# Optimization experiments

Measured on AMD Instinct MI355X. Metric: run time of the kernel, lower is better.

The kernel has to match this reference:

```python
import jax, jax.numpy as jnp
import numpy as np

B, S, H = 2, 1024, 4096
NH, NKV, D = 32, 8, 128
EPS = 1e-6
THETA = 10000.0


def rotate_half(x):
    x1, x2 = jnp.split(x, 2, axis=-1)
    return jnp.concatenate([-x2, x1], axis=-1)


def rmsnorm(x, w, eps):
    # RMSNorm over the last (head_dim) axis
    var = jnp.mean(x * x, axis=-1, keepdims=True)
    return x * jax.lax.rsqrt(var + eps) * w


def setup_inputs() -> dict:
    key = jax.random.key(0)
    ks = jax.random.split(key, 6)
    hidden_states = jax.random.normal(ks[0], (B, S, H), dtype=jnp.float32)
    # scaled init so activations stay O(1)
    Wq = jax.random.normal(ks[1], (NH * D, H), dtype=jnp.float32) * (H ** -0.5)
    Wk = jax.random.normal(ks[2], (NKV * D, H), dtype=jnp.float32) * (H ** -0.5)
    Wv = jax.random.normal(ks[3], (NKV * D, H), dtype=jnp.float32) * (H ** -0.5)
    Wo = jax.random.normal(ks[4], (H, NH * D), dtype=jnp.float32) * ((NH * D) ** -0.5)
    q_norm_w = jnp.ones((D,), dtype=jnp.float32)
    k_norm_w = jnp.ones((D,), dtype=jnp.float32)
    # standard default RoPE cos/sin tables, broadcast to [B, S, D]
    pos = jnp.arange(S, dtype=jnp.float32)
    inv_freq = 1.0 / (THETA ** (jnp.arange(0, D, 2, dtype=jnp.float32) / D))
    freqs = pos[:, None] * inv_freq[None, :]            # [S, D/2]
    emb = jnp.concatenate([freqs, freqs], axis=-1)      # [S, D]
    cos = jnp.broadcast_to(jnp.cos(emb)[None], (B, S, D)).astype(jnp.float32)
    sin = jnp.broadcast_to(jnp.sin(emb)[None], (B, S, D)).astype(jnp.float32)
    return dict(hidden_states=hidden_states, cos=cos, sin=sin,
                Wq=Wq, Wk=Wk, Wv=Wv, Wo=Wo,
                q_norm_w=q_norm_w, k_norm_w=k_norm_w)


def reference(hidden_states, cos, sin, Wq, Wk, Wv, Wo, q_norm_w, k_norm_w):
    b, s, h = hidden_states.shape
    # fused QKV projections (MojoLinear: y = x @ W.T, no bias)
    q = (hidden_states @ Wq.T).reshape(b, s, NH, D)
    k = (hidden_states @ Wk.T).reshape(b, s, NKV, D)
    v = (hidden_states @ Wv.T).reshape(b, s, NKV, D)
    # per-head-dim RMSNorm on q and k, then [B, H, S, D] layout
    q = rmsnorm(q, q_norm_w, EPS).transpose(0, 2, 1, 3)   # [B, NH,  S, D]
    k = rmsnorm(k, k_norm_w, EPS).transpose(0, 2, 1, 3)   # [B, NKV, S, D]
    v = v.transpose(0, 2, 1, 3)                           # [B, NKV, S, D]
    # RoPE (rotate-half)
    c = cos[:, None, :, :]
    sn = sin[:, None, :, :]
    q = q * c + rotate_half(q) * sn
    k = k * c + rotate_half(k) * sn
    # GQA: expand KV heads to query heads
    groups = NH // NKV
    k = jnp.repeat(k, groups, axis=1)                     # [B, NH, S, D]
    v = jnp.repeat(v, groups, axis=1)
    # causal attention (prefill with empty paged cache == causal SDPA)
    scores = jnp.einsum('bhqd,bhkd->bhqk', q, k) * (D ** -0.5)
    causal = jnp.tril(jnp.ones((s, s), dtype=bool))
    scores = jnp.where(causal, scores, jnp.finfo(scores.dtype).min)
    probs = jax.nn.softmax(scores, axis=-1)
    out = jnp.einsum('bhqk,bhkd->bhqd', probs, v)         # [B, NH, S, D]
    out = out.transpose(0, 2, 1, 3).reshape(b, s, NH * D)
    return out @ Wo.T
```

## Files before the change

kernel.cpp:

```cpp
#include <hip/hip_runtime.h>


typedef float  f32x4   __attribute__((ext_vector_type(4)));
typedef float  f32x16  __attribute__((ext_vector_type(16)));
typedef __bf16 bf16x8  __attribute__((ext_vector_type(8)));
typedef unsigned short u16x8 __attribute__((ext_vector_type(8)));

__device__ __forceinline__ unsigned short f2b(float f) {
    union { float f; unsigned int u; } x;
    x.f = f;
    unsigned int u = x.u;
    unsigned int r = u + 0x7fffu + ((u >> 16) & 1u);
    return (unsigned short)(r >> 16);
}
__device__ __forceinline__ float b2f(unsigned short h) {
    union { unsigned int u; float f; } x;
    x.u = ((unsigned int)h) << 16;
    return x.f;
}

__device__ __forceinline__ void async16(const unsigned short* g, unsigned short* l) {
    __builtin_amdgcn_global_load_lds(
        (const __attribute__((address_space(1))) void*)g,
        (__attribute__((address_space(3))) void*)l, 16, 0, 0);
}

__global__ __launch_bounds__(256) void cvt_pack(const float* __restrict__ hid,
                                                const float* __restrict__ Wq,
                                                const float* __restrict__ Wk,
                                                const float* __restrict__ Wv,
                                                const float* __restrict__ Wo,
                                                unsigned short* __restrict__ hidb,
                                                unsigned short* __restrict__ Wqkvb,
                                                unsigned short* __restrict__ Wob) {
    __shared__ __align__(16) unsigned short L[8192];
    const int t = threadIdx.x;
    const int tile = blockIdx.x;

    const float* src;
    unsigned short* dst;
    int kb;
    if (tile < 1024) {
        int rb = tile >> 6; kb = tile & 63;
        src = hid + (size_t)rb * 128 * 4096;
        dst = hidb + (size_t)tile * 8192;
    } else if (tile < 4096) {
        int tt = tile - 1024;
        int rb = tt >> 6; kb = tt & 63;
        dst = Wqkvb + (size_t)tt * 8192;
        if (rb < 32)      src = Wq + (size_t)rb * 128 * 4096;
        else if (rb < 40) src = Wk + (size_t)(rb - 32) * 128 * 4096;
        else              src = Wv + (size_t)(rb - 40) * 128 * 4096;
    } else {
        int tt = tile - 4096;
        int rb = tt >> 6; kb = tt & 63;
        src = Wo + (size_t)rb * 128 * 4096;
        dst = Wob + (size_t)tt * 8192;
    }

    const int r0 = t >> 2, cq = t & 3;
    #pragma unroll
    for (int rr = 0; rr < 2; rr++) {
        int row = r0 + rr * 64;
        const float* sp = src + (size_t)row * 4096 + kb * 64 + cq * 16;
        float4 v0 = ((const float4*)sp)[0];
        float4 v1 = ((const float4*)sp)[1];
        float4 v2 = ((const float4*)sp)[2];
        float4 v3 = ((const float4*)sp)[3];
        u16x8 a, b;
        a[0]=f2b(v0.x); a[1]=f2b(v0.y); a[2]=f2b(v0.z); a[3]=f2b(v0.w);
        a[4]=f2b(v1.x); a[5]=f2b(v1.y); a[6]=f2b(v1.z); a[7]=f2b(v1.w);
        b[0]=f2b(v2.x); b[1]=f2b(v2.y); b[2]=f2b(v2.z); b[3]=f2b(v2.w);
        b[4]=f2b(v3.x); b[5]=f2b(v3.y); b[6]=f2b(v3.z); b[7]=f2b(v3.w);
        *(u16x8*)&L[((cq * 2)     * 128 + row) * 8] = a;
        *(u16x8*)&L[((cq * 2 + 1) * 128 + row) * 8] = b;
    }
    __syncthreads();
    #pragma unroll
    for (int j = 0; j < 4; j++)
        *(u16x8*)(dst + t * 32 + j * 8) = *(const u16x8*)&L[t * 32 + j * 8];
}

template<bool BF16OUT>
__global__ __launch_bounds__(256) void gemm_packed(const unsigned short* __restrict__ A,
                                                   const unsigned short* __restrict__ W,
                                                   void* __restrict__ Cv,
                                                   int K, int N) {
    __shared__ __align__(16) unsigned short As[8192];
    __shared__ __align__(16) unsigned short Bs[8192];

    const int tid  = threadIdx.x;
    const int wave = tid >> 6, lane = tid & 63;
    const int wm   = wave >> 1, wn = wave & 1;
    const int l31  = lane & 31, lh = lane >> 5;
    const int KT   = K >> 6;

    const unsigned short* Ap = A + (size_t)blockIdx.y * KT * 8192;
    const unsigned short* Wp = W + (size_t)blockIdx.x * KT * 8192;

    f32x16 acc[2][2] = {};

    for (int kt = 0; kt < KT; kt++) {
        const unsigned short* at = Ap + (size_t)kt * 8192;
        const unsigned short* wt = Wp + (size_t)kt * 8192;
        #pragma unroll
        for (int it = 0; it < 4; it++) {
            int slot = it * 4 + wave;
            async16(at + slot * 512 + lane * 8, &As[slot * 512]);
            async16(wt + slot * 512 + lane * 8, &Bs[slot * 512]);
        }
        __syncthreads();

        bf16x8 af[4][2], bfr[4][2];
        #pragma unroll
        for (int ks = 0; ks < 4; ks++) {
            #pragma unroll
            for (int i = 0; i < 2; i++) {
                int ch = ks * 2 + lh;
                af[ks][i]  = *(const bf16x8*)&As[(ch * 128 + wm * 64 + i * 32 + l31) * 8];
                bfr[ks][i] = *(const bf16x8*)&Bs[(ch * 128 + wn * 64 + i * 32 + l31) * 8];
            }
        }
        #pragma unroll
        for (int ks = 0; ks < 4; ks++)
            #pragma unroll
            for (int i = 0; i < 2; i++)
                #pragma unroll
                for (int j = 0; j < 2; j++)
                    acc[i][j] = __builtin_amdgcn_mfma_f32_32x32x16_bf16(af[ks][i], bfr[ks][j], acc[i][j], 0, 0, 0);
        __syncthreads();
    }

    const int arow = blockIdx.y * 128, brow = blockIdx.x * 128;
    #pragma unroll
    for (int i = 0; i < 2; i++)
        #pragma unroll
        for (int j = 0; j < 2; j++)
            #pragma unroll
            for (int r = 0; r < 16; r++) {
                int row = arow + wm * 64 + i * 32 + lh * 4 + (r & 3) + 8 * (r >> 2);
                int col = brow + wn * 64 + j * 32 + l31;
                if (BF16OUT)
                    ((unsigned short*)Cv)[(size_t)row * N + col] = f2b(acc[i][j][r]);
                else
                    ((float*)Cv)[(size_t)row * N + col] = acc[i][j][r];
            }
}

__global__ __launch_bounds__(256) void norm_rope_qk(const unsigned short* __restrict__ X,
                                                    const float* __restrict__ cosp,
                                                    const float* __restrict__ sinp,
                                                    const float* __restrict__ qw,
                                                    const float* __restrict__ kw,
                                                    unsigned short* __restrict__ Qb,
                                                    unsigned short* __restrict__ Kb) {
    const int wid  = blockIdx.x * 4 + (threadIdx.x >> 6);
    const int lane = threadIdx.x & 63;

    const unsigned short* xp;
    const float* w;
    unsigned short* yp;
    int row;
    if (wid < 65536) {
        row = wid >> 5;
        int h = wid & 31;
        xp = X + (size_t)row * 6144 + h * 128;
        w  = qw;
        yp = Qb + (((size_t)((row >> 10) * 32 + h)) * 1024 + (row & 1023)) * 128;
    } else {
        int wid2 = wid - 65536;
        row = wid2 >> 3;
        int h = wid2 & 7;
        xp = X + (size_t)row * 6144 + 4096 + h * 128;
        w  = kw;
        yp = Kb + (((size_t)((row >> 10) * 8 + h)) * 1024 + (row & 1023)) * 128;
    }

    float x0 = b2f(xp[lane]), x1 = b2f(xp[lane + 64]);
    float ss = x0 * x0 + x1 * x1;
    #pragma unroll
    for (int off = 32; off; off >>= 1) ss += __shfl_xor(ss, off, 64);
    float r = rsqrtf(ss * (1.0f / 128.0f) + 1e-6f);
    float n0 = x0 * r * w[lane];
    float n1 = x1 * r * w[lane + 64];
    const float* cp = cosp + (size_t)row * 128;
    const float* sp = sinp + (size_t)row * 128;
    float y0 = n0 * cp[lane]      - n1 * sp[lane];
    float y1 = n1 * cp[lane + 64] + n0 * sp[lane + 64];
    yp[lane]      = f2b(y0);
    yp[lane + 64] = f2b(y1);
}

__global__ __launch_bounds__(256) void v_trans(const unsigned short* __restrict__ V,
                                               unsigned short* __restrict__ Vt) {
    __shared__ unsigned short T[64][68];
    const int tid = threadIdx.x;
    const int st = blockIdx.x >> 1, dt = blockIdx.x & 1;
    const int bh = blockIdx.y, b = bh >> 3, h = bh & 7;

    const int sl = tid >> 2, c0 = (tid & 3) * 16;
    const unsigned short* src = V + (size_t)(b * 1024 + st * 64 + sl) * 6144 + h * 128 + dt * 64 + c0;
    *(u16x8*)&T[sl][c0]     = *(const u16x8*)(src);
    *(u16x8*)&T[sl][c0 + 8] = *(const u16x8*)(src + 8);
    __syncthreads();

    const int dgrp = tid >> 6, sl2 = tid & 63;
    unsigned short* dst = Vt + (size_t)bh * 131072 + st * 64 + sl2;
    #pragma unroll
    for (int jd = 0; jd < 16; jd++) {
        int dl = dgrp * 16 + jd;
        dst[(size_t)(dt * 64 + dl) * 1024] = T[sl2][dl];
    }
}

__global__ __launch_bounds__(256) void attn(const unsigned short* __restrict__ Qb,
                                            const unsigned short* __restrict__ Kb,
                                            const unsigned short* __restrict__ Vt,
                                            unsigned short* __restrict__ Ob) {
    __shared__ __align__(16) unsigned short Klds[128 * 128];
    __shared__ __align__(16) unsigned short Plds[4][16][136];

    const int tid  = threadIdx.x;
    const int w    = tid >> 6, lane = tid & 63;
    const int quad = lane >> 4, l15 = lane & 15;
    const int h = blockIdx.y, b = blockIdx.z, kvh = h >> 2;

    const unsigned short* Qp = Qb + ((size_t)(b * 32 + h))   * 131072;
    const unsigned short* Kp = Kb + ((size_t)(b * 8 + kvh))  * 131072;
    const unsigned short* Vp = Vt + ((size_t)(b * 8 + kvh))  * 131072;
    const float c2 = (float)(0.08838834764831845 * 1.4426950408889634);

    for (int half = 0; half < 2; half++) {
        const int qt = half ? (15 - (int)blockIdx.x) : (int)blockIdx.x;
        const int q0 = qt * 64;
        const int qrow = q0 + w * 16 + l15;

        bf16x8 qf[4];
        #pragma unroll
        for (int ks = 0; ks < 4; ks++)
            qf[ks] = *(const bf16x8*)(Qp + (size_t)qrow * 128 + ks * 32 + quad * 8);

        float l_i[4] = {0.0f, 0.0f, 0.0f, 0.0f};
        f32x4 o[8] = {};

        const int ntiles = (qt >> 1) + 1;
        const int nfull  = (qt * 64 + 1) >> 7;

        for (int kt = 0; kt < ntiles; kt++) {
            __syncthreads();
            #pragma unroll
            for (int it = 0; it < 8; it++) {
                int slot = it * 4 + w;
                int ci = slot * 64 + lane;
                int r = ci >> 4, c = ci & 15;
                int g = (c & 8) | ((c ^ r) & 7);
                async16(Kp + (size_t)(kt * 128 + r) * 128 + g * 8, &Klds[slot * 512]);
            }
            __syncthreads();

            f32x4 sacc[8] = {};
            #pragma unroll
            for (int ks = 0; ks < 4; ks++) {
                #pragma unroll
                for (int tn = 0; tn < 8; tn++) {
                    int row = tn * 16 + l15;
                    int ch  = ks * 4 + quad;
                    int chs = (ch & 8) | ((ch ^ row) & 7);
                    bf16x8 kf = *(const bf16x8*)&Klds[row * 128 + chs * 8];
                    sacc[tn] = __builtin_amdgcn_mfma_f32_16x16x32_bf16(qf[ks], kf, sacc[tn], 0, 0, 0);
                }
            }

            const bool masked = (kt >= nfull);
            #pragma unroll
            for (int r = 0; r < 4; r++) {
                const int qg = q0 + w * 16 + quad * 4 + r;
                #pragma unroll
                for (int tn = 0; tn < 8; tn++) {
                    float p = __builtin_amdgcn_exp2f(sacc[tn][r] * c2 - 17.0f);
                    if (masked && (kt * 128 + tn * 16 + l15 > qg)) p = 0.0f;
                    l_i[r] += p;
                    Plds[w][quad * 4 + r][tn * 16 + l15] = f2b(p);
                }
            }

            #pragma unroll
            for (int ks = 0; ks < 4; ks++) {
                bf16x8 pf = *(const bf16x8*)&Plds[w][l15][ks * 32 + quad * 8];
                #pragma unroll
                for (int td = 0; td < 8; td++) {
                    bf16x8 vf = *(const bf16x8*)(Vp + (size_t)(td * 16 + l15) * 1024 + kt * 128 + ks * 32 + quad * 8);
                    o[td] = __builtin_amdgcn_mfma_f32_16x16x32_bf16(pf, vf, o[td], 0, 0, 0);
                }
            }
        }

        #pragma unroll
        for (int r = 0; r < 4; r++) {
            float l = l_i[r];
            #pragma unroll
            for (int off = 8; off; off >>= 1) l += __shfl_xor(l, off, 16);
            float inv = 1.0f / l;
            const int qg = q0 + w * 16 + quad * 4 + r;
            const int rowg = b * 1024 + qg;
            const int rb = rowg >> 7, rloc = rowg & 127;
            #pragma unroll
            for (int td = 0; td < 8; td++) {
                int colg = h * 128 + td * 16 + l15;
                size_t cell = ((size_t)(rb * 64 + (colg >> 6)) * 1024 + ((colg >> 3) & 7) * 128 + rloc);
                Ob[cell * 8 + (colg & 7)] = f2b(o[td][r] * inv);
            }
        }
    }
}

extern "C" void kernel_launch(void* const* d_in, const int* in_sizes, int n_in,
                              void* d_out, int out_size, void* d_ws, size_t ws_size,
                              hipStream_t stream) {
    const float* hid  = (const float*)d_in[0];
    const float* cosp = (const float*)d_in[1];
    const float* sinp = (const float*)d_in[2];
    const float* Wq   = (const float*)d_in[3];
    const float* Wk   = (const float*)d_in[4];
    const float* Wv   = (const float*)d_in[5];
    const float* Wo   = (const float*)d_in[6];
    const float* qw   = (const float*)d_in[7];
    const float* kw   = (const float*)d_in[8];
    float* out = (float*)d_out;

    char* ws = (char*)d_ws;
    unsigned short* QKVb = (unsigned short*)ws;
    unsigned short* Ob   = QKVb;
    size_t off = (size_t)2048 * 6144 * 2;
    unsigned short* hidb  = (unsigned short*)(ws + off); off += (size_t)2048 * 4096 * 2;
    unsigned short* Wqkvb = (unsigned short*)(ws + off); off += (size_t)6144 * 4096 * 2;
    unsigned short* Wob   = (unsigned short*)(ws + off); off += (size_t)4096 * 4096 * 2;
    unsigned short* Qb    = (unsigned short*)(ws + off); off += (size_t)2048 * 4096 * 2;
    unsigned short* Kb    = (unsigned short*)(ws + off); off += (size_t)2048 * 1024 * 2;
    unsigned short* Vt    = (unsigned short*)(ws + off);

    dim3 blk(256);
    cvt_pack<<<6144, blk, 0, stream>>>(hid, Wq, Wk, Wv, Wo, hidb, Wqkvb, Wob);
    gemm_packed<true><<<dim3(48, 16), blk, 0, stream>>>(hidb, Wqkvb, QKVb, 4096, 6144);
    norm_rope_qk<<<20480, blk, 0, stream>>>(QKVb, cosp, sinp, qw, kw, Qb, Kb);
    v_trans<<<dim3(32, 16), blk, 0, stream>>>(QKVb + 5120, Vt);
    attn<<<dim3(8, 32, 2), blk, 0, stream>>>(Qb, Kb, Vt, Ob);
    gemm_packed<false><<<dim3(32, 16), blk, 0, stream>>>(Ob, Wob, out, 4096, 4096);
}
```

Measured before the change: 527.6 us.

## Fuse Q RMSNorm and RoPE into attention prologue, drop causal tile pairing

Q normalization and rotary embedding now run inside the attention kernel, which reads raw bf16 Q straight from the QKV buffer. This removes the intermediate Qb write and read and shrinks the norm kernel to K heads only. The attention grid changes from 8 blocks each handling a paired short and long query tile to 16 blocks with one tile each, which gives up the causal load balancing. Ob moves to its own buffer instead of aliasing QKVb, since QKVb is now still being read during attention.

```diff
diff --git a/kernel.cpp b/kernel.cpp
--- a/kernel.cpp
+++ b/kernel.cpp
@@ -82,10 +82,9 @@
 }
 
 template<bool BF16OUT>
-__global__ __launch_bounds__(256) void gemm_packed(const unsigned short* __restrict__ A,
-                                                   const unsigned short* __restrict__ W,
-                                                   void* __restrict__ Cv,
-                                                   int K, int N) {
+__device__ __forceinline__ void gemm_body(const unsigned short* __restrict__ A,
+                                          const unsigned short* __restrict__ W,
+                                          void* __restrict__ Cv, int K, int N) {
     __shared__ __align__(16) unsigned short As[8192];
     __shared__ __align__(16) unsigned short Bs[8192];
 
@@ -147,46 +146,42 @@
             }
 }
 
-__global__ __launch_bounds__(256) void norm_rope_qk(const unsigned short* __restrict__ X,
-                                                    const float* __restrict__ cosp,
-                                                    const float* __restrict__ sinp,
-                                                    const float* __restrict__ qw,
-                                                    const float* __restrict__ kw,
-                                                    unsigned short* __restrict__ Qb,
-                                                    unsigned short* __restrict__ Kb) {
+__global__ __launch_bounds__(256) void qkv_gemm(const unsigned short* __restrict__ A,
+                                                const unsigned short* __restrict__ W,
+                                                unsigned short* __restrict__ C,
+                                                int K, int N) {
+    gemm_body<true>(A, W, C, K, N);
+}
+__global__ __launch_bounds__(256) void out_gemm(const unsigned short* __restrict__ A,
+                                                const unsigned short* __restrict__ W,
+                                                float* __restrict__ C,
+                                                int K, int N) {
+    gemm_body<false>(A, W, C, K, N);
+}
+
+__global__ __launch_bounds__(256) void norm_rope_k(const unsigned short* __restrict__ X,
+                                                   const float* __restrict__ cosp,
+                                                   const float* __restrict__ sinp,
+                                                   const float* __restrict__ kw,
+                                                   unsigned short* __restrict__ Kb) {
     const int wid  = blockIdx.x * 4 + (threadIdx.x >> 6);
     const int lane = threadIdx.x & 63;
-
-    const unsigned short* xp;
-    const float* w;
-    unsigned short* yp;
-    int row;
-    if (wid < 65536) {
-        row = wid >> 5;
-        int h = wid & 31;
-        xp = X + (size_t)row * 6144 + h * 128;
-        w  = qw;
-        yp = Qb + (((size_t)((row >> 10) * 32 + h)) * 1024 + (row & 1023)) * 128;
-    } else {
-        int wid2 = wid - 65536;
-        row = wid2 >> 3;
-        int h = wid2 & 7;
-        xp = X + (size_t)row * 6144 + 4096 + h * 128;
-        w  = kw;
-        yp = Kb + (((size_t)((row >> 10) * 8 + h)) * 1024 + (row & 1023)) * 128;
-    }
-
+    const int row  = wid >> 3;
+    const int h    = wid & 7;
+
+    const unsigned short* xp = X + (size_t)row * 6144 + 4096 + h * 128;
     float x0 = b2f(xp[lane]), x1 = b2f(xp[lane + 64]);
     float ss = x0 * x0 + x1 * x1;
     #pragma unroll
     for (int off = 32; off; off >>= 1) ss += __shfl_xor(ss, off, 64);
     float r = rsqrtf(ss * (1.0f / 128.0f) + 1e-6f);
-    float n0 = x0 * r * w[lane];
-    float n1 = x1 * r * w[lane + 64];
+    float n0 = x0 * r * kw[lane];
+    float n1 = x1 * r * kw[lane + 64];
     const float* cp = cosp + (size_t)row * 128;
     const float* sp = sinp + (size_t)row * 128;
     float y0 = n0 * cp[lane]      - n1 * sp[lane];
     float y1 = n1 * cp[lane + 64] + n0 * sp[lane + 64];
+    unsigned short* yp = Kb + (((size_t)((row >> 10) * 8 + h)) * 1024 + (row & 1023)) * 128;
     yp[lane]      = f2b(y0);
     yp[lane + 64] = f2b(y1);
 }
@@ -213,7 +208,10 @@
     }
 }
 
-__global__ __launch_bounds__(256) void attn(const unsigned short* __restrict__ Qb,
+__global__ __launch_bounds__(256) void attn(const unsigned short* __restrict__ X,
+                                            const float* __restrict__ cosp,
+                                            const float* __restrict__ sinp,
+                                            const float* __restrict__ qw,
                                             const unsigned short* __restrict__ Kb,
                                             const unsigned short* __restrict__ Vt,
                                             unsigned short* __restrict__ Ob) {
@@ -223,93 +221,120 @@
     const int tid  = threadIdx.x;
     const int w    = tid >> 6, lane = tid & 63;
     const int quad = lane >> 4, l15 = lane & 15;
-    const int h = blockIdx.y, b = blockIdx.z, kvh = h >> 2;
-
-    const unsigned short* Qp = Qb + ((size_t)(b * 32 + h))   * 131072;
-    const unsigned short* Kp = Kb + ((size_t)(b * 8 + kvh))  * 131072;
-    const unsigned short* Vp = Vt + ((size_t)(b * 8 + kvh))  * 131072;
+    const int qt = blockIdx.x, h = blockIdx.y, b = blockIdx.z, kvh = h >> 2;
+
+    const unsigned short* Kp = Kb + ((size_t)(b * 8 + kvh)) * 131072;
+    const unsigned short* Vp = Vt + ((size_t)(b * 8 + kvh)) * 131072;
     const float c2 = (float)(0.08838834764831845 * 1.4426950408889634);
 
-    for (int half = 0; half < 2; half++) {
-        const int qt = half ? (15 - (int)blockIdx.x) : (int)blockIdx.x;
-        const int q0 = qt * 64;
-        const int qrow = q0 + w * 16 + l15;
-
-        bf16x8 qf[4];
-        #pragma unroll
-        for (int ks = 0; ks < 4; ks++)
-            qf[ks] = *(const bf16x8*)(Qp + (size_t)qrow * 128 + ks * 32 + quad * 8);
-
-        float l_i[4] = {0.0f, 0.0f, 0.0f, 0.0f};
-        f32x4 o[8] = {};
-
-        const int ntiles = (qt >> 1) + 1;
-        const int nfull  = (qt * 64 + 1) >> 7;
-
-        for (int kt = 0; kt < ntiles; kt++) {
-            __syncthreads();
-            #pragma unroll
-            for (int it = 0; it < 8; it++) {
-                int slot = it * 4 + w;
-                int ci = slot * 64 + lane;
-                int r = ci >> 4, c = ci & 15;
-                int g = (c & 8) | ((c ^ r) & 7);
-                async16(Kp + (size_t)(kt * 128 + r) * 128 + g * 8, &Klds[slot * 512]);
-            }
-            __syncthreads();
-
-            f32x4 sacc[8] = {};
-            #pragma unroll
-            for (int ks = 0; ks < 4; ks++) {
-                #pragma unroll
-                for (int tn = 0; tn < 8; tn++) {
-                    int row = tn * 16 + l15;
-                    int ch  = ks * 4 + quad;
-                    int chs = (ch & 8) | ((ch ^ row) & 7);
-                    bf16x8 kf = *(const bf16x8*)&Klds[row * 128 + chs * 8];
-                    sacc[tn] = __builtin_amdgcn_mfma_f32_16x16x32_bf16(qf[ks], kf, sacc[tn], 0, 0, 0);
-                }
-            }
-
-            const bool masked = (kt >= nfull);
-            #pragma unroll
-            for (int r = 0; r < 4; r++) {
-                const int qg = q0 + w * 16 + quad * 4 + r;
-                #pragma unroll
-                for (int tn = 0; tn < 8; tn++) {
-                    float p = __builtin_amdgcn_exp2f(sacc[tn][r] * c2 - 17.0f);
-                    if (masked && (kt * 128 + tn * 16 + l15 > qg)) p = 0.0f;
-                    l_i[r] += p;
-                    Plds[w][quad * 4 + r][tn * 16 + l15] = f2b(p);
-                }
-            }
-
-            #pragma unroll
-            for (int ks = 0; ks < 4; ks++) {
-                bf16x8 pf = *(const bf16x8*)&Plds[w][l15][ks * 32 + quad * 8];
-                #pragma unroll
-                for (int td = 0; td < 8; td++) {
-                    bf16x8 vf = *(const bf16x8*)(Vp + (size_t)(td * 16 + l15) * 1024 + kt * 128 + ks * 32 + quad * 8);
-                    o[td] = __builtin_amdgcn_mfma_f32_16x16x32_bf16(pf, vf, o[td], 0, 0, 0);
-                }
-            }
-        }
-
+    const int q0 = qt * 64;
+    const int qrow = q0 + w * 16 + l15;
+
+    const unsigned short* xp = X + (size_t)(b * 1024 + qrow) * 6144 + h * 128;
+    float nv[4][8];
+    float ss = 0.0f;
+    #pragma unroll
+    for (int ks = 0; ks < 4; ks++) {
+        u16x8 xv = *(const u16x8*)(xp + ks * 32 + quad * 8);
+        #pragma unroll
+        for (int j = 0; j < 8; j++) { float f = b2f(xv[j]); nv[ks][j] = f; ss += f * f; }
+    }
+    ss += __shfl_xor(ss, 16, 64);
+    ss += __shfl_xor(ss, 32, 64);
+    const float rn = rsqrtf(ss * (1.0f / 128.0f) + 1e-6f);
+    #pragma unroll
+    for (int ks = 0; ks < 4; ks++) {
+        const float4* wp4 = (const float4*)(qw + ks * 32 + quad * 8);
+        float4 w0 = wp4[0], w1 = wp4[1];
+        nv[ks][0] *= rn * w0.x; nv[ks][1] *= rn * w0.y; nv[ks][2] *= rn * w0.z; nv[ks][3] *= rn * w0.w;
+        nv[ks][4] *= rn * w1.x; nv[ks][5] *= rn * w1.y; nv[ks][6] *= rn * w1.z; nv[ks][7] *= rn * w1.w;
+    }
+    const float* cp = cosp + (size_t)(b * 1024 + qrow) * 128;
+    const float* sp = sinp + (size_t)(b * 1024 + qrow) * 128;
+    bf16x8 qf[4];
+    #pragma unroll
+    for (int ks = 0; ks < 4; ks++) {
+        const float4* c4 = (const float4*)(cp + ks * 32 + quad * 8);
+        const float4* s4 = (const float4*)(sp + ks * 32 + quad * 8);
+        float4 ca = c4[0], cb = c4[1], sa = s4[0], sb = s4[1];
+        float cc[8] = {ca.x, ca.y, ca.z, ca.w, cb.x, cb.y, cb.z, cb.w};
+        float sn[8] = {sa.x, sa.y, sa.z, sa.w, sb.x, sb.y, sb.z, sb.w};
+        #pragma unroll
+        for (int j = 0; j < 8; j++) {
+            float pair = (ks < 2) ? -nv[ks + 2][j] : nv[ks - 2][j];
+            qf[ks][j] = (__bf16)(nv[ks][j] * cc[j] + pair * sn[j]);
+        }
+    }
+
+    float l_i[4] = {0.0f, 0.0f, 0.0f, 0.0f};
+    f32x4 o[8] = {};
+
+    const int ntiles = (qt >> 1) + 1;
+    const int nfull  = (qt * 64 + 1) >> 7;
+
+    for (int kt = 0; kt < ntiles; kt++) {
+        __syncthreads();
+        #pragma unroll
+        for (int it = 0; it < 8; it++) {
+            int slot = it * 4 + w;
+            int ci = slot * 64 + lane;
+            int r = ci >> 4, c = ci & 15;
+            int g = (c & 8) | ((c ^ r) & 7);
+            async16(Kp + (size_t)(kt * 128 + r) * 128 + g * 8, &Klds[slot * 512]);
+        }
+        __syncthreads();
+
+        f32x4 sacc[8] = {};
+        #pragma unroll
+        for (int ks = 0; ks < 4; ks++) {
+            #pragma unroll
+            for (int tn = 0; tn < 8; tn++) {
+                int row = tn * 16 + l15;
+                int ch  = ks * 4 + quad;
+                int chs = (ch & 8) | ((ch ^ row) & 7);
+                bf16x8 kf = *(const bf16x8*)&Klds[row * 128 + chs * 8];
+                sacc[tn] = __builtin_amdgcn_mfma_f32_16x16x32_bf16(qf[ks], kf, sacc[tn], 0, 0, 0);
+            }
+        }
+
+        const bool masked = (kt >= nfull);
         #pragma unroll
         for (int r = 0; r < 4; r++) {
-            float l = l_i[r];
-            #pragma unroll
-            for (int off = 8; off; off >>= 1) l += __shfl_xor(l, off, 16);
-            float inv = 1.0f / l;
             const int qg = q0 + w * 16 + quad * 4 + r;
-            const int rowg = b * 1024 + qg;
-            const int rb = rowg >> 7, rloc = rowg & 127;
+            #pragma unroll
+            for (int tn = 0; tn < 8; tn++) {
+                float p = __builtin_amdgcn_exp2f(sacc[tn][r] * c2 - 17.0f);
+                if (masked && (kt * 128 + tn * 16 + l15 > qg)) p = 0.0f;
+                l_i[r] += p;
+                Plds[w][quad * 4 + r][tn * 16 + l15] = f2b(p);
+            }
+        }
+
+        #pragma unroll
+        for (int ks = 0; ks < 4; ks++) {
+            bf16x8 pf = *(const bf16x8*)&Plds[w][l15][ks * 32 + quad * 8];
             #pragma unroll
             for (int td = 0; td < 8; td++) {
-                int colg = h * 128 + td * 16 + l15;
-                size_t cell = ((size_t)(rb * 64 + (colg >> 6)) * 1024 + ((colg >> 3) & 7) * 128 + rloc);
-                Ob[cell * 8 + (colg & 7)] = f2b(o[td][r] * inv);
-            }
+                bf16x8 vf = *(const bf16x8*)(Vp + (size_t)(td * 16 + l15) * 1024 + kt * 128 + ks * 32 + quad * 8);
+                o[td] = __builtin_amdgcn_mfma_f32_16x16x32_bf16(pf, vf, o[td], 0, 0, 0);
+            }
+        }
+    }
+
+    #pragma unroll
+    for (int r = 0; r < 4; r++) {
+        float l = l_i[r];
+        #pragma unroll
+        for (int off = 8; off; off >>= 1) l += __shfl_xor(l, off, 16);
+        float inv = 1.0f / l;
+        const int qg = q0 + w * 16 + quad * 4 + r;
+        const int rowg = b * 1024 + qg;
+        const int rb = rowg >> 7, rloc = rowg & 127;
+        #pragma unroll
+        for (int td = 0; td < 8; td++) {
+            int colg = h * 128 + td * 16 + l15;
+            size_t cell = ((size_t)(rb * 64 + (colg >> 6)) * 1024 + ((colg >> 3) & 7) * 128 + rloc);
+            Ob[cell * 8 + (colg & 7)] = f2b(o[td][r] * inv);
         }
     }
 }
@@ -330,20 +355,19 @@
 
     char* ws = (char*)d_ws;
     unsigned short* QKVb = (unsigned short*)ws;
-    unsigned short* Ob   = QKVb;
     size_t off = (size_t)2048 * 6144 * 2;
     unsigned short* hidb  = (unsigned short*)(ws + off); off += (size_t)2048 * 4096 * 2;
     unsigned short* Wqkvb = (unsigned short*)(ws + off); off += (size_t)6144 * 4096 * 2;
     unsigned short* Wob   = (unsigned short*)(ws + off); off += (size_t)4096 * 4096 * 2;
-    unsigned short* Qb    = (unsigned short*)(ws + off); off += (size_t)2048 * 4096 * 2;
     unsigned short* Kb    = (unsigned short*)(ws + off); off += (size_t)2048 * 1024 * 2;
-    unsigned short* Vt    = (unsigned short*)(ws + off);
+    unsigned short* Vt    = (unsigned short*)(ws + off); off += (size_t)2048 * 1024 * 2;
+    unsigned short* Ob    = (unsigned short*)(ws + off);
 
     dim3 blk(256);
     cvt_pack<<<6144, blk, 0, stream>>>(hid, Wq, Wk, Wv, Wo, hidb, Wqkvb, Wob);
-    gemm_packed<true><<<dim3(48, 16), blk, 0, stream>>>(hidb, Wqkvb, QKVb, 4096, 6144);
-    norm_rope_qk<<<20480, blk, 0, stream>>>(QKVb, cosp, sinp, qw, kw, Qb, Kb);
+    qkv_gemm<<<dim3(48, 16), blk, 0, stream>>>(hidb, Wqkvb, QKVb, 4096, 6144);
+    norm_rope_k<<<4096, blk, 0, stream>>>(QKVb, cosp, sinp, kw, Kb);
     v_trans<<<dim3(32, 16), blk, 0, stream>>>(QKVb + 5120, Vt);
-    attn<<<dim3(8, 32, 2), blk, 0, stream>>>(Qb, Kb, Vt, Ob);
-    gemm_packed<false><<<dim3(32, 16), blk, 0, stream>>>(Ob, Wob, out, 4096, 4096);
-}
+    attn<<<dim3(16, 32, 2), blk, 0, stream>>>(QKVb, cosp, sinp, qw, Kb, Vt, Ob);
+    out_gemm<<<dim3(32, 16), blk, 0, stream>>>(Ob, Wob, out, 4096, 4096);
+}
```

Measured after the change: 603.9 us. 1.14x slower.
